# Kernel tuning notes

Hardware: AMD Instinct MI355X
Metric: run time of the kernel (lower is better)

## Reference

```python
import jax, jax.numpy as jnp
import numpy as np

N_NODES = 50000
N_EDGES = 800000
IN_DIM = 128
HEADS = 4
HID = 32
NEG_SLOPE = 0.2


def setup_inputs() -> dict:
    key = jax.random.key(0)
    ks = jax.random.split(key, 10)

    def glorot(k, shape, fan):
        return jax.random.normal(k, shape, jnp.float32) * (1.0 / np.sqrt(fan))

    x = jax.random.normal(ks[0], (N_NODES, IN_DIM), jnp.float32)
    edge_index = jax.random.randint(ks[1], (2, N_EDGES), 0, N_NODES)
    # layer 1: in=IN_DIM, out=HEADS*HID (concat)
    Wl1 = glorot(ks[2], (IN_DIM, HEADS * HID), IN_DIM)
    Wr1 = glorot(ks[3], (IN_DIM, HEADS * HID), IN_DIM)
    att1 = glorot(ks[4], (HEADS, HID), HID)
    b1 = jnp.zeros((HEADS * HID,), jnp.float32)
    # layer 2: in=HEADS*HID, out=HID (mean over heads)
    Wl2 = glorot(ks[5], (HEADS * HID, HEADS * HID), HEADS * HID)
    Wr2 = glorot(ks[6], (HEADS * HID, HEADS * HID), HEADS * HID)
    att2 = glorot(ks[7], (HEADS, HID), HID)
    b2 = jnp.zeros((HID,), jnp.float32)
    return {"x": x, "edge_index": edge_index, "Wl1": Wl1, "Wr1": Wr1,
            "att1": att1, "b1": b1, "Wl2": Wl2, "Wr2": Wr2,
            "att2": att2, "b2": b2}


def _gatv2_conv(x, src, dst, Wl, Wr, att, bias, concat):
    """PyG GATv2Conv (eval mode, self loops already in src/dst)."""
    n = x.shape[0]
    h, c = att.shape
    xl = (x @ Wl).reshape(n, h, c)  # source transform
    xr = (x @ Wr).reshape(n, h, c)  # destination transform
    e = jax.nn.leaky_relu(xl[src] + xr[dst], NEG_SLOPE)   # [E, H, C]
    logits = jnp.einsum('ehc,hc->eh', e, att)             # [E, H]
    # segment softmax over edges grouped by destination node
    m = jax.ops.segment_max(logits, dst, num_segments=n)  # [N, H]
    a = jnp.exp(logits - m[dst])
    denom = jax.ops.segment_sum(a, dst, num_segments=n)   # [N, H]
    alpha = a / denom[dst]                                # [E, H]
    out = jax.ops.segment_sum(xl[src] * alpha[..., None], dst,
                              num_segments=n)             # [N, H, C]
    out = out.reshape(n, h * c) if concat else out.mean(axis=1)
    return out + bias


def reference(x, edge_index, Wl1, Wr1, att1, b1, Wl2, Wr2, att2, b2):
    n = x.shape[0]
    loop = jnp.arange(n, dtype=edge_index.dtype)
    src = jnp.concatenate([edge_index[0], loop])
    dst = jnp.concatenate([edge_index[1], loop])
    h1 = jax.nn.relu(_gatv2_conv(x, src, dst, Wl1, Wr1, att1, b1, concat=True))
    h2 = jax.nn.relu(_gatv2_conv(h1, src, dst, Wl2, Wr2, att2, b2, concat=False))
    return h2
```

## Files before the change

kernel.cpp:

```cpp
#include <hip/hip_runtime.h>
#include <hip/hip_bf16.h>
#include <hip/hip_fp16.h>

#define HEADS 4
#define HID 32
#define DIM 128
#define CAP 64

typedef __attribute__((ext_vector_type(8))) short bf16x8;
typedef __attribute__((ext_vector_type(4))) float f32x4;

__device__ __forceinline__ float bf2f(unsigned short u) {
    return __uint_as_float(((unsigned int)u) << 16);
}
__device__ __forceinline__ unsigned short f2bf(float f) {
    unsigned int u = __float_as_uint(f);
    unsigned int r = u + 0x7fffu + ((u >> 16) & 1u);
    return (unsigned short)(r >> 16);
}
__device__ __forceinline__ float dload(const float* f, const unsigned short* b, int isb, size_t i) {
    return isb ? bf2f(b[i]) : f[i];
}
__device__ __forceinline__ float2 h2f2(unsigned int u) {
    __half2 h = *(__half2*)&u;
    return make_float2(__low2float(h), __high2float(h));
}

__global__ void detect_dtype(const unsigned short* __restrict__ xu, int* __restrict__ flag)
{
    int tid = threadIdx.x;
    float v = bf2f(xu[tid * 2]);
    float av = fabsf(v);
    int sane = (v == v && av > 1e-4f && av < 1e4f) ? 1 : 0;
    __shared__ int cnt;
    if (tid == 0) cnt = 0;
    __syncthreads();
    atomicAdd(&cnt, sane);
    __syncthreads();
    if (tid == 0) *flag = (cnt >= 128) ? 1 : 0;
}

__device__ __forceinline__ void wprep_block(int blk,
                      const float* __restrict__ Wlf, const unsigned short* __restrict__ Wlb,
                      const float* __restrict__ Wrf, const unsigned short* __restrict__ Wrb,
                      int isb, uint4* __restrict__ wf)
{
    const int gtid = blk * 256 + threadIdx.x;
    const int lane = gtid & 63;
    const int ks = (gtid >> 6) & 3;
    const int nt = gtid >> 8;
    const int col = nt * 16 + (lane & 15);
    const int kbase = ks * 32 + (lane >> 4) * 8;
    unsigned short hs[8], ls[8];
#pragma unroll
    for (int j = 0; j < 8; ++j) {
        int k = kbase + j;
        float w = (col < 128) ? dload(Wlf, Wlb, isb, (size_t)k * 128 + col)
                              : dload(Wrf, Wrb, isb, (size_t)k * 128 + col - 128);
        hs[j] = f2bf(w);
        ls[j] = f2bf(w - bf2f(hs[j]));
    }
    uint4 H, L;
    H.x = hs[0] | ((unsigned)hs[1] << 16); H.y = hs[2] | ((unsigned)hs[3] << 16);
    H.z = hs[4] | ((unsigned)hs[5] << 16); H.w = hs[6] | ((unsigned)hs[7] << 16);
    L.x = ls[0] | ((unsigned)ls[1] << 16); L.y = ls[2] | ((unsigned)ls[3] << 16);
    L.z = ls[4] | ((unsigned)ls[5] << 16); L.w = ls[6] | ((unsigned)ls[7] << 16);
    wf[((0 * 16 + nt) * 4 + ks) * 64 + lane] = H;
    wf[((1 * 16 + nt) * 4 + ks) * 64 + lane] = L;
}

__global__ void prep(int* __restrict__ cnt, int N, int ZB, const int* __restrict__ flag,
                     const float* Wl1f, const unsigned short* Wl1b,
                     const float* Wr1f, const unsigned short* Wr1b, uint4* __restrict__ wf1,
                     const float* Wl2f, const unsigned short* Wl2b,
                     const float* Wr2f, const unsigned short* Wr2b, uint4* __restrict__ wf2)
{
    int b = blockIdx.x;
    if (b < ZB) {
        int i = b * 256 + threadIdx.x;
        if (i < N) cnt[i] = 0;
        return;
    }
    const int isb = *flag;
    b -= ZB;
    if (b < 16) wprep_block(b, Wl1f, Wl1b, Wr1f, Wr1b, isb, wf1);
    else        wprep_block(b - 16, Wl2f, Wl2b, Wr2f, Wr2b, isb, wf2);
}

__global__ void scatter_edges(const int* __restrict__ ei, int E,
                              int* __restrict__ cnt, int* __restrict__ bucket)
{
    int e = blockIdx.x * blockDim.x + threadIdx.x;
    if (e < E) {
        int s = ei[e], d = ei[E + e];
        int slot = atomicAdd(&cnt[d], 1);
        if (slot < CAP) bucket[(size_t)d * CAP + slot] = s;
    }
}

template<bool X_DUAL>
__global__ void __launch_bounds__(256, 2)
mfma_gemm(const float* __restrict__ xf, const unsigned short* __restrict__ xb,
          const uint4* __restrict__ wf, const int* __restrict__ flag,
          unsigned short* __restrict__ xlh, float* __restrict__ xr, int N)
{
    const int isb = *flag;
    const int tid = threadIdx.x;
    const int base = blockIdx.x * 64;
    __shared__ uint4 ldsA[2 * 4 * 4 * 64];

#pragma unroll
    for (int it = 0; it < 4; ++it) {
        int t = tid + it * 256;
        int r = t >> 4, kb = t & 15;
        int row = base + r;
        float v[8];
        if (row < N) {
            size_t idx = (size_t)row * DIM + kb * 8;
            if (X_DUAL && isb) {
#pragma unroll
                for (int j = 0; j < 8; ++j) v[j] = bf2f(xb[idx + j]);
            } else {
                float4 p0 = *(const float4*)(xf + idx);
                float4 p1 = *(const float4*)(xf + idx + 4);
                v[0] = p0.x; v[1] = p0.y; v[2] = p0.z; v[3] = p0.w;
                v[4] = p1.x; v[5] = p1.y; v[6] = p1.z; v[7] = p1.w;
            }
        } else {
#pragma unroll
            for (int j = 0; j < 8; ++j) v[j] = 0.f;
        }
        unsigned short hs[8], ls[8];
#pragma unroll
        for (int j = 0; j < 8; ++j) {
            hs[j] = f2bf(v[j]);
            ls[j] = f2bf(v[j] - bf2f(hs[j]));
        }
        uint4 H, L;
        H.x = hs[0] | ((unsigned)hs[1] << 16); H.y = hs[2] | ((unsigned)hs[3] << 16);
        H.z = hs[4] | ((unsigned)hs[5] << 16); H.w = hs[6] | ((unsigned)hs[7] << 16);
        L.x = ls[0] | ((unsigned)ls[1] << 16); L.y = ls[2] | ((unsigned)ls[3] << 16);
        L.z = ls[4] | ((unsigned)ls[5] << 16); L.w = ls[6] | ((unsigned)ls[7] << 16);
        int mtile = r >> 4, kstep = kb >> 2, lane = (kb & 3) * 16 + (r & 15);
        ldsA[((0 * 4 + mtile) * 4 + kstep) * 64 + lane] = H;
        ldsA[((1 * 4 + mtile) * 4 + kstep) * 64 + lane] = L;
    }
    __syncthreads();

    const int w = tid >> 6, lane = tid & 63;
    const int nloc = lane & 15;
    const int e0 = (lane >> 4) << 2;

#pragma unroll 2
    for (int ntq = 0; ntq < 4; ++ntq) {
        const int nt = w * 4 + ntq;
        bf16x8 bh[4], bl[4];
#pragma unroll
        for (int ks = 0; ks < 4; ++ks) {
            bh[ks] = *(const bf16x8*)&wf[((0 * 16 + nt) * 4 + ks) * 64 + lane];
            bl[ks] = *(const bf16x8*)&wf[((1 * 16 + nt) * 4 + ks) * 64 + lane];
        }
#pragma unroll
        for (int mt = 0; mt < 4; ++mt) {
            f32x4 a0 = {0.f, 0.f, 0.f, 0.f};
            f32x4 a1 = {0.f, 0.f, 0.f, 0.f};
            f32x4 a2 = {0.f, 0.f, 0.f, 0.f};
#pragma unroll
            for (int ks = 0; ks < 4; ++ks) {
                bf16x8 ah = *(bf16x8*)&ldsA[((0 * 4 + mt) * 4 + ks) * 64 + lane];
                bf16x8 al = *(bf16x8*)&ldsA[((1 * 4 + mt) * 4 + ks) * 64 + lane];
                a0 = __builtin_amdgcn_mfma_f32_16x16x32_bf16(ah, bh[ks], a0, 0, 0, 0);
                a1 = __builtin_amdgcn_mfma_f32_16x16x32_bf16(al, bh[ks], a1, 0, 0, 0);
                a2 = __builtin_amdgcn_mfma_f32_16x16x32_bf16(ah, bl[ks], a2, 0, 0, 0);
            }
            f32x4 acc = a0 + a1 + a2;
            const int r0 = base + mt * 16 + e0;
            if (nt < 8) {
                const int col = nt * 16 + nloc;
#pragma unroll
                for (int e = 0; e < 4; ++e) {
                    int row = r0 + e;
                    if (row < N) xlh[(size_t)row * DIM + col] = __half_as_ushort(__float2half(acc[e]));
                }
            } else {
                const int col = nt * 16 + nloc - 128;
#pragma unroll
                for (int e = 0; e < 4; ++e) {
                    int row = r0 + e;
                    if (row < N) xr[(size_t)row * DIM + col] = acc[e];
                }
            }
        }
    }
}

template<int LAYER>
__global__ void fused_node(const unsigned short* __restrict__ xlh, const float* __restrict__ xr,
                           const int* __restrict__ bucket, const int* __restrict__ cnt,
                           const float* __restrict__ attf, const unsigned short* __restrict__ attb,
                           const float* __restrict__ bf_, const unsigned short* __restrict__ bb,
                           const int* __restrict__ flag, int N, void* __restrict__ outp)
{
    const int node = blockIdx.x * 4 + (threadIdx.x >> 6);
    if (node >= N) return;
    const int l = threadIdx.x & 63;
    const int isb = *flag;
    const unsigned int* xl2 = (const unsigned int*)xlh;

    const float att0 = dload(attf, attb, isb, 2 * l);
    const float att1 = dload(attf, attb, isb, 2 * l + 1);
    const float2 rv = *(const float2*)(xr + (size_t)node * DIM + 2 * l);

    int deg = cnt[node];
    deg = deg < CAP ? deg : CAP;
    const int m = deg + 1;
    const int* bk = bucket + (size_t)node * CAP;

    const int myslot = (l < deg) ? bk[l] : node;
#define SRCOF(J) ((J) < deg ? __shfl(myslot, (J) & 63) : node)

    unsigned int b[4];
#pragma unroll
    for (int p = 0; p < 4; ++p) b[p] = xl2[(size_t)SRCOF(p) * 64 + l];

    float num0 = 0.f, num1 = 0.f, den = 0.f;
    const int mfull = m & ~3;
    for (int j = 0; j < mfull; j += 4) {
#pragma unroll
        for (int p = 0; p < 4; ++p) {
            float2 v = h2f2(b[p]);
            b[p] = xl2[(size_t)SRCOF(j + 4 + p) * 64 + l];
            float u0 = v.x + rv.x, u1 = v.y + rv.y;
            float t = fmaf(att0, fmaf(0.2f, fminf(u0, 0.f), fmaxf(u0, 0.f)),
                           att1 * fmaf(0.2f, fminf(u1, 0.f), fmaxf(u1, 0.f)));
#pragma unroll
            for (int off = 1; off < 16; off <<= 1) t += __shfl_xor(t, off);
            float a = __expf(fminf(fmaxf(t, -50.f), 50.f));
            den += a;
            num0 = fmaf(a, v.x, num0);
            num1 = fmaf(a, v.y, num1);
        }
    }
    const int rem = m - mfull;
    if (rem) {
#pragma unroll
        for (int p = 0; p < 4; ++p) {
            if (p < rem) {
                float2 v = h2f2(b[p]);
                float u0 = v.x + rv.x, u1 = v.y + rv.y;
                float t = fmaf(att0, fmaf(0.2f, fminf(u0, 0.f), fmaxf(u0, 0.f)),
                               att1 * fmaf(0.2f, fminf(u1, 0.f), fmaxf(u1, 0.f)));
#pragma unroll
                for (int off = 1; off < 16; off <<= 1) t += __shfl_xor(t, off);
                float a = __expf(fminf(fmaxf(t, -50.f), 50.f));
                den += a;
                num0 = fmaf(a, v.x, num0);
                num1 = fmaf(a, v.y, num1);
            }
        }
    }
#undef SRCOF
    float o0 = num0 / den, o1 = num1 / den;

    if (LAYER == 1) {
        float w0 = o0 + dload(bf_, bb, isb, 2 * l);
        float w1 = o1 + dload(bf_, bb, isb, 2 * l + 1);
        float2 st = make_float2(w0 > 0.f ? w0 : 0.f, w1 > 0.f ? w1 : 0.f);
        *(float2*)((float*)outp + (size_t)node * DIM + 2 * l) = st;
    } else {
        float s0v = o0, s1v = o1;
        s0v += __shfl_xor(s0v, 16); s0v += __shfl_xor(s0v, 32);
        s1v += __shfl_xor(s1v, 16); s1v += __shfl_xor(s1v, 32);
        if (l < 16) {
            float v0 = 0.25f * s0v + dload(bf_, bb, isb, 2 * l);
            float v1 = 0.25f * s1v + dload(bf_, bb, isb, 2 * l + 1);
            v0 = v0 > 0.f ? v0 : 0.f;
            v1 = v1 > 0.f ? v1 : 0.f;
            if (isb) {
                unsigned int pk = (unsigned int)f2bf(v0) | ((unsigned int)f2bf(v1) << 16);
                *(unsigned int*)((unsigned short*)outp + (size_t)node * HID + 2 * l) = pk;
            } else {
                *(float2*)((float*)outp + (size_t)node * HID + 2 * l) = make_float2(v0, v1);
            }
        }
    }
}

extern "C" void kernel_launch(void* const* d_in, const int* in_sizes, int n_in,
                              void* d_out, int out_size, void* d_ws, size_t ws_size,
                              hipStream_t stream)
{
#define DUAL(i) (const float*)d_in[i], (const unsigned short*)d_in[i]
    const int* ei = (const int*)d_in[1];

    const int N = in_sizes[0] / DIM;
    const int E = in_sizes[1] / 2;

    float* ws = (float*)d_ws;
    const size_t NF = (size_t)N * DIM;
    unsigned short* f_xlh = (unsigned short*)ws;
    float* f_xr   = ws + NF / 2;
    float* f_h1   = f_xr + NF;
    int*   bucket = (int*)(f_h1 + NF);
    int*   cnt    = bucket + (size_t)N * CAP;
    int*   flag   = cnt + N;
    size_t wf_off = ((size_t)(flag + 1) - (size_t)d_ws + 15) & ~(size_t)15;
    uint4* wfrag1 = (uint4*)((char*)d_ws + wf_off);
    uint4* wfrag2 = wfrag1 + 8192;

    const dim3 B(256);
    const int gemm_blocks = (N + 63) / 64;
    const int node_blocks = (N + 3) / 4;
    const int ZB = (N + 255) / 256;

    detect_dtype<<<1, B, 0, stream>>>((const unsigned short*)d_in[0], flag);

    prep<<<ZB + 32, B, 0, stream>>>(cnt, N, ZB, flag,
                                    DUAL(2), DUAL(3), wfrag1,
                                    DUAL(6), DUAL(7), wfrag2);
    scatter_edges<<<(E + 255) / 256, B, 0, stream>>>(ei, E, cnt, bucket);

    mfma_gemm<true><<<gemm_blocks, B, 0, stream>>>(DUAL(0), wfrag1, flag, f_xlh, f_xr, N);
    fused_node<1><<<node_blocks, B, 0, stream>>>(f_xlh, f_xr, bucket, cnt, DUAL(4), DUAL(5),
                                                 flag, N, f_h1);

    mfma_gemm<false><<<gemm_blocks, B, 0, stream>>>(f_h1, nullptr, wfrag2, flag, f_xlh, f_xr, N);
    fused_node<2><<<node_blocks, B, 0, stream>>>(f_xlh, f_xr, bucket, cnt, DUAL(8), DUAL(9),
                                                 flag, N, d_out);
#undef DUAL
}
```

Measured before the change: 291.1 us.

## Fuse edge scatter into layer-1 GEMM launch and restructure weight-fragment loading

The edge bucketing kernel is merged into the first GEMM launch as extra blocks, so the scatter runs alongside the GEMM and one launch disappears. The GEMM n-tile loop is restructured to load weight fragments for two n-tiles at once, with an outer loop that is not unrolled, which changes register pressure and load scheduling. LeakyReLU is simplified to max(u, 0.2u). The fused scatter blocks share the GEMM's launch bounds, and their atomics may contend with GEMM memory traffic.

```diff
diff --git a/kernel.cpp b/kernel.cpp
--- a/kernel.cpp
+++ b/kernel.cpp
@@ -87,23 +87,24 @@
     else        wprep_block(b - 16, Wl2f, Wl2b, Wr2f, Wr2b, isb, wf2);
 }
 
-__global__ void scatter_edges(const int* __restrict__ ei, int E,
-                              int* __restrict__ cnt, int* __restrict__ bucket)
-{
-    int e = blockIdx.x * blockDim.x + threadIdx.x;
-    if (e < E) {
-        int s = ei[e], d = ei[E + e];
-        int slot = atomicAdd(&cnt[d], 1);
-        if (slot < CAP) bucket[(size_t)d * CAP + slot] = s;
-    }
-}
-
 template<bool X_DUAL>
 __global__ void __launch_bounds__(256, 2)
 mfma_gemm(const float* __restrict__ xf, const unsigned short* __restrict__ xb,
           const uint4* __restrict__ wf, const int* __restrict__ flag,
-          unsigned short* __restrict__ xlh, float* __restrict__ xr, int N)
-{
+          unsigned short* __restrict__ xlh, float* __restrict__ xr, int N,
+          int gemmBlocks, const int* __restrict__ ei, int E,
+          int* __restrict__ cnt, int* __restrict__ bucket)
+{
+    if ((int)blockIdx.x >= gemmBlocks) {
+        int e = ((int)blockIdx.x - gemmBlocks) * 256 + threadIdx.x;
+        if (e < E) {
+            int s = ei[e], d = ei[E + e];
+            int slot = atomicAdd(&cnt[d], 1);
+            if (slot < CAP) bucket[(size_t)d * CAP + slot] = s;
+        }
+        return;
+    }
+
     const int isb = *flag;
     const int tid = threadIdx.x;
     const int base = blockIdx.x * 64;
@@ -151,43 +152,50 @@
     const int nloc = lane & 15;
     const int e0 = (lane >> 4) << 2;
 
-#pragma unroll 2
-    for (int ntq = 0; ntq < 4; ++ntq) {
-        const int nt = w * 4 + ntq;
-        bf16x8 bh[4], bl[4];
-#pragma unroll
-        for (int ks = 0; ks < 4; ++ks) {
-            bh[ks] = *(const bf16x8*)&wf[((0 * 16 + nt) * 4 + ks) * 64 + lane];
-            bl[ks] = *(const bf16x8*)&wf[((1 * 16 + nt) * 4 + ks) * 64 + lane];
-        }
-#pragma unroll
-        for (int mt = 0; mt < 4; ++mt) {
-            f32x4 a0 = {0.f, 0.f, 0.f, 0.f};
-            f32x4 a1 = {0.f, 0.f, 0.f, 0.f};
-            f32x4 a2 = {0.f, 0.f, 0.f, 0.f};
+#pragma unroll 1
+    for (int half = 0; half < 2; ++half) {
+        bf16x8 bh[2][4], bl[2][4];
+#pragma unroll
+        for (int sub = 0; sub < 2; ++sub) {
+            const int nt = w * 4 + half * 2 + sub;
 #pragma unroll
             for (int ks = 0; ks < 4; ++ks) {
-                bf16x8 ah = *(bf16x8*)&ldsA[((0 * 4 + mt) * 4 + ks) * 64 + lane];
-                bf16x8 al = *(bf16x8*)&ldsA[((1 * 4 + mt) * 4 + ks) * 64 + lane];
-                a0 = __builtin_amdgcn_mfma_f32_16x16x32_bf16(ah, bh[ks], a0, 0, 0, 0);
-                a1 = __builtin_amdgcn_mfma_f32_16x16x32_bf16(al, bh[ks], a1, 0, 0, 0);
-                a2 = __builtin_amdgcn_mfma_f32_16x16x32_bf16(ah, bl[ks], a2, 0, 0, 0);
-            }
-            f32x4 acc = a0 + a1 + a2;
-            const int r0 = base + mt * 16 + e0;
-            if (nt < 8) {
-                const int col = nt * 16 + nloc;
-#pragma unroll
-                for (int e = 0; e < 4; ++e) {
-                    int row = r0 + e;
-                    if (row < N) xlh[(size_t)row * DIM + col] = __half_as_ushort(__float2half(acc[e]));
+                bh[sub][ks] = *(const bf16x8*)&wf[((0 * 16 + nt) * 4 + ks) * 64 + lane];
+                bl[sub][ks] = *(const bf16x8*)&wf[((1 * 16 + nt) * 4 + ks) * 64 + lane];
+            }
+        }
+#pragma unroll
+        for (int sub = 0; sub < 2; ++sub) {
+            const int nt = w * 4 + half * 2 + sub;
+#pragma unroll
+            for (int mt = 0; mt < 4; ++mt) {
+                f32x4 a0 = {0.f, 0.f, 0.f, 0.f};
+                f32x4 a1 = {0.f, 0.f, 0.f, 0.f};
+                f32x4 a2 = {0.f, 0.f, 0.f, 0.f};
+#pragma unroll
+                for (int ks = 0; ks < 4; ++ks) {
+                    bf16x8 ah = *(bf16x8*)&ldsA[((0 * 4 + mt) * 4 + ks) * 64 + lane];
+                    bf16x8 al = *(bf16x8*)&ldsA[((1 * 4 + mt) * 4 + ks) * 64 + lane];
+                    a0 = __builtin_amdgcn_mfma_f32_16x16x32_bf16(ah, bh[sub][ks], a0, 0, 0, 0);
+                    a1 = __builtin_amdgcn_mfma_f32_16x16x32_bf16(al, bh[sub][ks], a1, 0, 0, 0);
+                    a2 = __builtin_amdgcn_mfma_f32_16x16x32_bf16(ah, bl[sub][ks], a2, 0, 0, 0);
                 }
-            } else {
-                const int col = nt * 16 + nloc - 128;
-#pragma unroll
-                for (int e = 0; e < 4; ++e) {
-                    int row = r0 + e;
-                    if (row < N) xr[(size_t)row * DIM + col] = acc[e];
+                f32x4 acc = a0 + a1 + a2;
+                const int r0 = base + mt * 16 + e0;
+                if (nt < 8) {
+                    const int col = nt * 16 + nloc;
+#pragma unroll
+                    for (int e = 0; e < 4; ++e) {
+                        int row = r0 + e;
+                        if (row < N) xlh[(size_t)row * DIM + col] = __half_as_ushort(__float2half(acc[e]));
+                    }
+                } else {
+                    const int col = nt * 16 + nloc - 128;
+#pragma unroll
+                    for (int e = 0; e < 4; ++e) {
+                        int row = r0 + e;
+                        if (row < N) xr[(size_t)row * DIM + col] = acc[e];
+                    }
                 }
             }
         }
@@ -231,8 +239,8 @@
             float2 v = h2f2(b[p]);
             b[p] = xl2[(size_t)SRCOF(j + 4 + p) * 64 + l];
             float u0 = v.x + rv.x, u1 = v.y + rv.y;
-            float t = fmaf(att0, fmaf(0.2f, fminf(u0, 0.f), fmaxf(u0, 0.f)),
-                           att1 * fmaf(0.2f, fminf(u1, 0.f), fmaxf(u1, 0.f)));
+            float t = fmaf(att0, fmaxf(u0, 0.2f * u0),
+                           att1 * fmaxf(u1, 0.2f * u1));
 #pragma unroll
             for (int off = 1; off < 16; off <<= 1) t += __shfl_xor(t, off);
             float a = __expf(fminf(fmaxf(t, -50.f), 50.f));
@@ -248,8 +256,8 @@
             if (p < rem) {
                 float2 v = h2f2(b[p]);
                 float u0 = v.x + rv.x, u1 = v.y + rv.y;
-                float t = fmaf(att0, fmaf(0.2f, fminf(u0, 0.f), fmaxf(u0, 0.f)),
-                               att1 * fmaf(0.2f, fminf(u1, 0.f), fmaxf(u1, 0.f)));
+                float t = fmaf(att0, fmaxf(u0, 0.2f * u0),
+                               att1 * fmaxf(u1, 0.2f * u1));
 #pragma unroll
                 for (int off = 1; off < 16; off <<= 1) t += __shfl_xor(t, off);
                 float a = __expf(fminf(fmaxf(t, -50.f), 50.f));
@@ -312,19 +320,21 @@
     const int gemm_blocks = (N + 63) / 64;
     const int node_blocks = (N + 3) / 4;
     const int ZB = (N + 255) / 256;
+    const int scat_blocks = (E + 255) / 256;
 
     detect_dtype<<<1, B, 0, stream>>>((const unsigned short*)d_in[0], flag);
 
     prep<<<ZB + 32, B, 0, stream>>>(cnt, N, ZB, flag,
                                     DUAL(2), DUAL(3), wfrag1,
                                     DUAL(6), DUAL(7), wfrag2);
-    scatter_edges<<<(E + 255) / 256, B, 0, stream>>>(ei, E, cnt, bucket);
-
-    mfma_gemm<true><<<gemm_blocks, B, 0, stream>>>(DUAL(0), wfrag1, flag, f_xlh, f_xr, N);
+
+    mfma_gemm<true><<<gemm_blocks + scat_blocks, B, 0, stream>>>(
+        DUAL(0), wfrag1, flag, f_xlh, f_xr, N, gemm_blocks, ei, E, cnt, bucket);
     fused_node<1><<<node_blocks, B, 0, stream>>>(f_xlh, f_xr, bucket, cnt, DUAL(4), DUAL(5),
                                                  flag, N, f_h1);
 
-    mfma_gemm<false><<<gemm_blocks, B, 0, stream>>>(f_h1, nullptr, wfrag2, flag, f_xlh, f_xr, N);
+    mfma_gemm<false><<<gemm_blocks, B, 0, stream>>>(
+        f_h1, nullptr, wfrag2, flag, f_xlh, f_xr, N, gemm_blocks, nullptr, 0, nullptr, nullptr);
     fused_node<2><<<node_blocks, B, 0, stream>>>(f_xlh, f_xr, bucket, cnt, DUAL(8), DUAL(9),
                                                  flag, N, d_out);
 #undef DUAL
```

After: 302.2 us. +3.8%, slower.
